# Kernel optimization log

Measured on AMD Instinct MI355X. Metric: run time of the kernel, lower is better.

## Reference

```python
import jax, jax.numpy as jnp
import numpy as np

N_HEAD = 8
D_HEAD = 32  # d_model=256 // n_head=8
SCALE = 1.0 / (D_HEAD ** 0.5)
CLIP = 10.0


def _rel_shift(x):
    # x: [qlen, klen, B, nh]; Transformer-XL relative shift along axis 1
    qlen, klen = x.shape[0], x.shape[1]
    zero_pad = jnp.zeros((qlen, 1) + x.shape[2:], dtype=x.dtype)
    x_pad = jnp.concatenate([zero_pad, x], axis=1)          # [qlen, klen+1, B, nh]
    x_pad = x_pad.reshape((klen + 1, qlen) + x.shape[2:])   # row-major reshape (torch .view)
    return x_pad[1:].reshape(x.shape)


def setup_inputs() -> dict:
    key = jax.random.key(0)
    ks = jax.random.split(key, 7)
    S, B, H = 1024, 8, 256
    return {
        "q": jax.random.normal(ks[0], (S, B, H), dtype=jnp.float32),
        "k": jax.random.normal(ks[1], (S, B, H), dtype=jnp.float32),
        "v": jax.random.normal(ks[2], (S, B, H), dtype=jnp.float32),
        "r": jax.random.normal(ks[3], (S, 1, H), dtype=jnp.float32),
        "bias_u": jax.random.normal(ks[4], (N_HEAD, D_HEAD), dtype=jnp.float32),
        "bias_v": jax.random.normal(ks[5], (N_HEAD, D_HEAD), dtype=jnp.float32),
        "mask": jax.random.randint(ks[6], (S, S, B), 0, 2).astype(jnp.bool_),
    }


def reference(q, k, v, r, bias_u, bias_v, mask):
    qlen, bsz = q.shape[0], q.shape[1]
    klen, rlen = k.shape[0], r.shape[0]
    q = q.reshape(qlen, bsz, N_HEAD, D_HEAD)
    k = k.reshape(klen, bsz, N_HEAD, D_HEAD)
    v = v.reshape(klen, bsz, N_HEAD, D_HEAD)
    r = r.reshape(rlen, N_HEAD, D_HEAD)

    AC = jnp.einsum('ibnd,jbnd->ijbn', q + bias_u, k)   # content term
    BD = jnp.einsum('ibnd,jnd->ijbn', q + bias_v, r)    # position term
    BD = _rel_shift(BD)

    score = (AC + BD) * SCALE
    score = CLIP * jnp.tanh(score)                      # clip > 0 path

    weight = jax.nn.softmax(score, axis=1)              # softmax over klen

    # mask is not None path: masked softmax of head-mean logits
    logits = score.mean(axis=-1)                        # [qlen, klen, B]
    logits = jnp.where(mask, -jnp.inf, logits)
    probs = jax.nn.softmax(logits, axis=1)

    out = jnp.einsum('ijbn,jbnd->ibnd', weight, v)
    out = out.reshape(qlen, bsz, N_HEAD * D_HEAD)
    return out, probs
```

## Files before the change

### kernel.cpp

```cpp
#include <hip/hip_runtime.h>
#include <hip/hip_fp16.h>

#define S 1024
#define B 8
#define NH 8
#define DH 32
#define HID 256
#define SCALEF 0.17677669529663687f

typedef __attribute__((ext_vector_type(8))) _Float16 f16x8;
typedef __attribute__((ext_vector_type(4))) _Float16 f16x4;
typedef __attribute__((ext_vector_type(4))) float f32x4;
#define MFMAH(a, b, c) __builtin_amdgcn_mfma_f32_16x16x32_f16(a, b, c, 0, 0, 0)

#define OFF_K   0
#define OFF_VT  2560
#define OFF_RL  5120
#define OFF_RH  10240
#define OFF_P   15360
#define LDS_HF  17920

#define C_E2  0.51006978f
#define C_PWA 14.42695041f
#define C_PWB -28.85390082f

__device__ __forceinline__ void cvtf16_4(const float4 x, _Float16* d) {
  f16x4 h;
  h.x = (_Float16)x.x; h.y = (_Float16)x.y; h.z = (_Float16)x.z; h.w = (_Float16)x.w;
  *(f16x4*)d = h;
}

__global__ __launch_bounds__(256)
void relattn_mfma_86028194939537(const float* __restrict__ q, const float* __restrict__ k,
                                 const float* __restrict__ v, const float* __restrict__ r,
                                 const float* __restrict__ bu, const float* __restrict__ bv,
                                 float* __restrict__ out, __half* __restrict__ sws) {
  __shared__ _Float16 sm[LDS_HF];
  const int t = threadIdx.x;
  const int lane = t & 63, w = t >> 6;
  const int quad = lane >> 4, jn = lane & 15;
  const int bid = blockIdx.x;
  const int b = bid & 7, it = (bid >> 3) & 15, n = bid >> 7;
  const int i0 = it << 6, iw0 = i0 + (w << 4);
  const int colq = quad << 3;
  const int i16 = i0 >> 4;

  const int jstage = t >> 3, dstage = (t & 7) << 2;
  const int jsw = jstage ^ ((t & 3) << 3);
  const int vcolsw = colq ^ (((jn >> 2) & 3) << 3);

  const int jtL_last = (i0 + 63) >> 5;
  const bool proH = (i0 <= 125);

  f16x8 qu_h, qu_l, qv_h, qv_l, qn_h, qn_l;
  {
    const float* bup = bu + n * DH + colq;
    const float* bvp = bv + n * DH + colq;
    const float* qp = q + (size_t)(iw0 + jn) * 2048 + b * HID + n * DH + colq;
    int r1 = iw0 + 1 + jn; if (r1 > S - 1) r1 = S - 1;
    const float* qp1 = q + (size_t)r1 * 2048 + b * HID + n * DH + colq;
#pragma unroll
    for (int e = 0; e < 8; ++e) {
      float xu = (qp[e] + bup[e]) * C_E2;
      float xv = (qp[e] + bvp[e]) * C_E2;
      float xn = (qp1[e] + bvp[e]) * C_E2;
      _Float16 h;
      h = (_Float16)xu; qu_h[e] = h; qu_l[e] = (_Float16)(xu - (float)h);
      h = (_Float16)xv; qv_h[e] = h; qv_l[e] = (_Float16)(xv - (float)h);
      h = (_Float16)xn; qn_h[e] = h; qn_l[e] = (_Float16)(xn - (float)h);
    }
  }

  f16x8 ones1;
#pragma unroll
  for (int e = 0; e < 8; ++e) ones1[e] = (_Float16)1.0f;

  __half* swsp = sws + (((size_t)(iw0 + jn) * 8 + b) * 8 + n) * 1024 + colq;

  f32x4 out0 = {0.f, 0.f, 0.f, 0.f}, out1 = {0.f, 0.f, 0.f, 0.f};
  f32x4 out_sum = {0.f, 0.f, 0.f, 0.f};

  {
    const size_t g = (size_t)jstage * 2048 + b * HID + n * DH + dstage;
    float4 kx = *(const float4*)(k + g);
    float4 vx = *(const float4*)(v + g);
    cvtf16_4(kx, &sm[OFF_K + jstage * 40 + dstage]);
    sm[OFF_VT + (dstage + 0) * 40 + jsw] = (_Float16)vx.x;
    sm[OFF_VT + (dstage + 1) * 40 + jsw] = (_Float16)vx.y;
    sm[OFF_VT + (dstage + 2) * 40 + jsw] = (_Float16)vx.z;
    sm[OFF_VT + (dstage + 3) * 40 + jsw] = (_Float16)vx.w;
  }
#pragma unroll
  for (int p = 0; p < 3; ++p) {
    int ti = 2 * p + (t >> 7), row = (t >> 3) & 15, d4 = (t & 7) << 2;
    {
      int kL = 60 - i16 + ti;
      int tg = (kL << 4) + row; tg = tg < 0 ? 0 : (tg > S - 1 ? S - 1 : tg);
      float4 rv = *(const float4*)(r + (size_t)tg * HID + n * DH + d4);
      int sl = (kL + 72) & 7;
      cvtf16_4(rv, &sm[OFF_RL + (sl * 16 + row) * 40 + d4]);
    }
    if (proH) {
      int kH = -i16 - 3 + ti;
      int tg = (kH << 4) - 17 + row; tg = tg < 0 ? 0 : (tg > S - 1 ? S - 1 : tg);
      float4 rv = *(const float4*)(r + (size_t)tg * HID + n * DH + d4);
      int sl = (kH + 72) & 7;
      cvtf16_4(rv, &sm[OFF_RH + (sl * 16 + row) * 40 + d4]);
    }
  }

  for (int jt = 0; jt < 32; ++jt) {
    const int j0 = jt << 5;
    __syncthreads();

    const bool doKV = (jt < 31);
    const bool doRL = (jt <= jtL_last);
    const bool doRH = (32 * jt >= i0 - 125);
    float4 kx, vx, rlv, rhv;
    int slL = 0, slH = 0;
    {
      if (doKV) {
        const size_t g = (size_t)(j0 + 32 + jstage) * 2048 + b * HID + n * DH + dstage;
        kx = *(const float4*)(k + g);
        vx = *(const float4*)(v + g);
      }
      const int ti = t >> 7, row = (t >> 3) & 15, d4r = (t & 7) << 2;
      if (doRL) {
        int kL = 66 + 2 * jt - i16 + ti;
        int tg = (kL << 4) + row; tg = tg < 0 ? 0 : (tg > S - 1 ? S - 1 : tg);
        rlv = *(const float4*)(r + (size_t)tg * HID + n * DH + d4r);
        slL = (kL + 72) & 7;
      }
      if (doRH) {
        int kH = 2 * jt - i16 + 3 + ti;
        int tg = (kH << 4) - 17 + row; tg = tg < 0 ? 0 : (tg > S - 1 ? S - 1 : tg);
        rhv = *(const float4*)(r + (size_t)tg * HID + n * DH + d4r);
        slH = (kH + 72) & 7;
      }
    }

    const int buf = (jt & 1) * 1280;
    const bool lowA = (j0 <= iw0 + 15);
    const bool highA = (j0 + 29 >= iw0);

    f32x4 ac0 = {0.f, 0.f, 0.f, 0.f}, ac1 = {0.f, 0.f, 0.f, 0.f};
    {
      f16x8 b0 = *(const f16x8*)&sm[OFF_K + buf + jn * 40 + colq];
      f16x8 b1 = *(const f16x8*)&sm[OFF_K + buf + (16 + jn) * 40 + colq];
      ac0 = MFMAH(qu_h, b0, ac0); ac0 = MFMAH(qu_l, b0, ac0);
      ac1 = MFMAH(qu_h, b1, ac1); ac1 = MFMAH(qu_l, b1, ac1);
    }

    f32x4 zl0 = {0.f,0.f,0.f,0.f}, zl1 = {0.f,0.f,0.f,0.f}, zl2 = {0.f,0.f,0.f,0.f};
    f32x4 zh0 = {0.f,0.f,0.f,0.f}, zh1 = {0.f,0.f,0.f,0.f}, zh2 = {0.f,0.f,0.f,0.f};
    if (lowA) {
#pragma unroll
      for (int z = 0; z < 3; ++z) {
        int kL = 63 - i16 - w + 2 * jt + z;
        int sl = (kL + 72) & 7;
        f16x8 rr = *(const f16x8*)&sm[OFF_RL + (sl * 16 + jn) * 40 + colq];
        f32x4 acc = {0.f, 0.f, 0.f, 0.f};
        acc = MFMAH(qv_h, rr, acc); acc = MFMAH(qv_l, rr, acc);
        if (z == 0) zl0 = acc; else if (z == 1) zl1 = acc; else zl2 = acc;
      }
    }
    if (highA) {
#pragma unroll
      for (int z = 0; z < 3; ++z) {
        int kH = 2 * jt - i16 - w + z;
        int sl = (kH + 72) & 7;
        f16x8 rr = *(const f16x8*)&sm[OFF_RH + (sl * 16 + jn) * 40 + colq];
        f32x4 acc = {0.f, 0.f, 0.f, 0.f};
        acc = MFMAH(qn_h, rr, acc); acc = MFMAH(qn_l, rr, acc);
        if (z == 0) zh0 = acc; else if (z == 1) zh1 = acc; else zh2 = acc;
      }
    }

#pragma unroll
    for (int g = 0; g < 4; ++g) {
      const int qr = (quad << 2) + g;
      const int c0 = 15 - qr + jn;
      const int src = (lane & 48) | (c0 & 15);
      const bool pred = (jn >= 15 - qr);
      float lo0 = 0.f, lo1 = 0.f, hv0 = 0.f, hv1 = 0.f;
      if (lowA) {
        float vA = pred ? zl0[g] : zl1[g];
        float vB = pred ? zl1[g] : zl2[g];
        lo0 = __shfl(vA, src, 64);
        lo1 = __shfl(vB, src, 64);
      }
      if (highA) {
        float vA = pred ? zh0[g] : zh1[g];
        float vB = pred ? zh1[g] : zh2[g];
        hv0 = __shfl(vA, src, 64);
        hv1 = __shfl(vB, src, 64);
      }
      const int dj0 = j0 + jn - iw0 - qr;
#pragma unroll
      for (int f = 0; f < 2; ++f) {
        const int dj = dj0 + (f << 4);
        const float bd = (dj <= 0) ? (f ? lo1 : lo0) : ((dj == 1) ? 0.f : (f ? hv1 : hv0));
        const float acv = f ? ac1[g] : ac0[g];
        const float s = acv + bd;
        const float e2 = __builtin_amdgcn_exp2f(s);
        const float tq = __builtin_amdgcn_rcpf(e2 + 1.f);
        const float pw = __builtin_amdgcn_exp2f(fmaf(tq, C_PWB, C_PWA));
        sm[OFF_P + w * 640 + qr * 40 + (f << 4) + jn] = (_Float16)pw;
      }
    }

    {
      f16x8 pa = *(const f16x8*)&sm[OFF_P + w * 640 + jn * 40 + colq];
      f16x8 v0 = *(const f16x8*)&sm[OFF_VT + buf + jn * 40 + vcolsw];
      f16x8 v1 = *(const f16x8*)&sm[OFF_VT + buf + (16 + jn) * 40 + vcolsw];
      out0 = MFMAH(pa, v0, out0);
      out1 = MFMAH(pa, v1, out1);
      out_sum = MFMAH(pa, ones1, out_sum);
      *(f16x8*)swsp = pa;
      swsp += 32;
    }

    {
      if (doKV) {
        const int nbuf = ((jt + 1) & 1) * 1280;
        cvtf16_4(kx, &sm[OFF_K + nbuf + jstage * 40 + dstage]);
        sm[OFF_VT + nbuf + (dstage + 0) * 40 + jsw] = (_Float16)vx.x;
        sm[OFF_VT + nbuf + (dstage + 1) * 40 + jsw] = (_Float16)vx.y;
        sm[OFF_VT + nbuf + (dstage + 2) * 40 + jsw] = (_Float16)vx.z;
        sm[OFF_VT + nbuf + (dstage + 3) * 40 + jsw] = (_Float16)vx.w;
      }
      const int row = (t >> 3) & 15, d4r = (t & 7) << 2;
      if (doRL) cvtf16_4(rlv, &sm[OFF_RL + (slL * 16 + row) * 40 + d4r]);
      if (doRH) cvtf16_4(rhv, &sm[OFF_RH + (slH * 16 + row) * 40 + d4r]);
    }
  }

#pragma unroll
  for (int g = 0; g < 4; ++g) {
    const float inv = 1.0f / out_sum[g];
    const int qr = (quad << 2) + g;
    float* op = out + (size_t)(iw0 + qr) * 2048 + b * HID + n * DH;
    op[jn] = out0[g] * inv;
    op[16 + jn] = out1[g] * inv;
  }
}

__global__ __launch_bounds__(1024)
void relattn_probs_86028194939537(const __half* __restrict__ sws, const int* __restrict__ mask,
                                  float* __restrict__ probs) {
  __shared__ _Float16 ebuf[8][1032];
  __shared__ unsigned char mb[9224];
  __shared__ float psum[8][4];
  __shared__ float binv[8];
  const int t = threadIdx.x;
  const int i = blockIdx.x;
  const int tj = t & 255, bg = t >> 8;
  const int j4 = tj << 2;
  const int wl = (t >> 6) & 3;

  {
    const int4* m4 = (const int4*)(mask + (size_t)i * 8192);
#pragma unroll
    for (int u = 0; u < 2; ++u) {
      int idx = t + (u << 10);
      int4 mv = m4[idx];
      int jj = idx >> 1, b0 = (idx & 1) << 2;
      mb[jj * 9 + b0 + 0] = (unsigned char)(mv.x != 0);
      mb[jj * 9 + b0 + 1] = (unsigned char)(mv.y != 0);
      mb[jj * 9 + b0 + 2] = (unsigned char)(mv.z != 0);
      mb[jj * 9 + b0 + 3] = (unsigned char)(mv.w != 0);
    }
  }
  __syncthreads();

#pragma unroll
  for (int bb = 0; bb < 2; ++bb) {
    const int b = (bg << 1) + bb;
    float a0 = 1.f, a1 = 1.f, a2 = 1.f, a3 = 1.f;
#pragma unroll
    for (int n = 0; n < 8; ++n) {
      f16x4 pv = *(const f16x4*)(sws + (((size_t)i * 8 + b) * 8 + n) * 1024 + j4);
      a0 *= (float)pv.x; a1 *= (float)pv.y; a2 *= (float)pv.z; a3 *= (float)pv.w;
    }
    float e0 = mb[(j4 + 0) * 9 + b] ? 0.f
             : __builtin_amdgcn_exp2f(0.125f * __builtin_amdgcn_logf(a0));
    float e1 = mb[(j4 + 1) * 9 + b] ? 0.f
             : __builtin_amdgcn_exp2f(0.125f * __builtin_amdgcn_logf(a1));
    float e2 = mb[(j4 + 2) * 9 + b] ? 0.f
             : __builtin_amdgcn_exp2f(0.125f * __builtin_amdgcn_logf(a2));
    float e3 = mb[(j4 + 3) * 9 + b] ? 0.f
             : __builtin_amdgcn_exp2f(0.125f * __builtin_amdgcn_logf(a3));
    f16x4 ev;
    ev.x = (_Float16)e0; ev.y = (_Float16)e1; ev.z = (_Float16)e2; ev.w = (_Float16)e3;
    *(f16x4*)&ebuf[b][j4] = ev;
    float s = ((float)ev.x + (float)ev.y) + ((float)ev.z + (float)ev.w);
#pragma unroll
    for (int off = 32; off > 0; off >>= 1) s += __shfl_xor(s, off, 64);
    if ((t & 63) == 0) psum[b][wl] = s;
  }
  __syncthreads();
  if (t < 8) binv[t] = 1.0f / (psum[t][0] + psum[t][1] + psum[t][2] + psum[t][3]);
  __syncthreads();
#pragma unroll
  for (int u = 0; u < 2; ++u) {
    int f0 = (t << 2) + (u << 12);
    float4 o;
    o.x = (float)ebuf[(f0 + 0) & 7][(f0 + 0) >> 3] * binv[(f0 + 0) & 7];
    o.y = (float)ebuf[(f0 + 1) & 7][(f0 + 1) >> 3] * binv[(f0 + 1) & 7];
    o.z = (float)ebuf[(f0 + 2) & 7][(f0 + 2) >> 3] * binv[(f0 + 2) & 7];
    o.w = (float)ebuf[(f0 + 3) & 7][(f0 + 3) >> 3] * binv[(f0 + 3) & 7];
    *(float4*)(probs + (size_t)i * 8192 + f0) = o;
  }
}

#define TI 8
#define TJ 8
#define NTILE (S / TJ)
#define KSTR 288
#define KOFF 0
#define VOFF (TJ * KSTR)
#define BAND (2 * TJ * KSTR)
#define PROWS (TI + TJ - 1)
#define BSTR 292
#define BVR (BAND + PROWS * BSTR)
#define BUKo (BVR + PROWS * 8)
#define LDS_FL (BUKo + 64)

__global__ __launch_bounds__(256, 2)
void relattn_main_fb(const float* __restrict__ q, const float* __restrict__ k,
                     const float* __restrict__ v, const float* __restrict__ r,
                     const float* __restrict__ bias_u, const float* __restrict__ bias_v,
                     const int* __restrict__ mask, float* __restrict__ out,
                     float* __restrict__ probs_raw, float* __restrict__ ws_logits, int use_ws) {
  __shared__ float smf[LDS_FL];
  const int t = threadIdx.x;
  const int n = t & 7;
  const int il = (t >> 3) & 7;
  const int jp = t >> 6;
  const int bid = blockIdx.x;
  const int b = bid & 7;
  const int i0 = (bid >> 3) * TI;
  const int i = i0 + il;
  float qq[DH], qn[DH];
  {
    const float4* qr = (const float4*)(q + (i * B + b) * HID + n * DH);
#pragma unroll
    for (int dd = 0; dd < 8; ++dd) {
      float4 a = qr[dd];
      qq[4*dd+0] = a.x; qq[4*dd+1] = a.y; qq[4*dd+2] = a.z; qq[4*dd+3] = a.w;
    }
    if (i + 1 < S) {
      const float4* q2 = (const float4*)(q + ((i + 1) * B + b) * HID + n * DH);
#pragma unroll
      for (int dd = 0; dd < 8; ++dd) {
        float4 a = q2[dd];
        qn[4*dd+0] = a.x; qn[4*dd+1] = a.y; qn[4*dd+2] = a.z; qn[4*dd+3] = a.w;
      }
    } else {
#pragma unroll
      for (int d = 0; d < DH; ++d) qn[d] = 0.f;
    }
  }
  float oacc[DH];
#pragma unroll
  for (int d = 0; d < DH; ++d) oacc[d] = 0.f;
  float lsum = 0.f;
  for (int jt = 0; jt < NTILE; ++jt) {
    const int j0 = jt * TJ;
    const int Pstar = i0 + (TI - 1) - j0;
    const int lowBase = S - TI + j0 - i0;
    const int upBase = j0 - i0 - (TI + 1);
    __syncthreads();
    {
      int u = t;
      int row = u >> 6, c = u & 63;
      int gofs = ((j0 + row) * B + b) * HID + c * 4;
      int lofs = row * KSTR + (c >> 3) * 36 + (c & 7) * 4;
      *(float4*)(smf + KOFF + lofs) = *(const float4*)(k + gofs);
      *(float4*)(smf + VOFF + lofs) = *(const float4*)(v + gofs);
      u = t + 256; row = u >> 6; c = u & 63;
      gofs = ((j0 + row) * B + b) * HID + c * 4;
      lofs = row * KSTR + (c >> 3) * 36 + (c & 7) * 4;
      *(float4*)(smf + KOFF + lofs) = *(const float4*)(k + gofs);
      *(float4*)(smf + VOFF + lofs) = *(const float4*)(v + gofs);
    }
    for (int u = t; u < PROWS * 64; u += 256) {
      int prow = u >> 6, c = u & 63;
      int trow = (prow <= Pstar) ? (lowBase + prow) : (upBase + prow);
      float4 val = make_float4(0.f, 0.f, 0.f, 0.f);
      if ((unsigned)trow < (unsigned)S) val = *(const float4*)(r + trow * HID + c * 4);
      *(float4*)(smf + BAND + prow * BSTR + (c >> 3) * 36 + (c & 7) * 4) = val;
    }
    if (t < 64 + PROWS * 8) {
      const float4 *bb, *src;
      int slot;
      bool zero = false;
      if (t < 64) {
        int jl = t >> 3, nn = t & 7;
        bb = (const float4*)(bias_u + nn * DH);
        src = (const float4*)(k + ((j0 + jl) * B + b) * HID + nn * DH);
        slot = BUKo + jl * 8 + nn;
      } else {
        int u2 = t - 64;
        int prow = u2 >> 3, nn = u2 & 7;
        int trow = (prow <= Pstar) ? (lowBase + prow) : (upBase + prow);
        bb = (const float4*)(bias_v + nn * DH);
        if ((unsigned)trow < (unsigned)S) src = (const float4*)(r + trow * HID + nn * DH);
        else { src = bb; zero = true; }
        slot = BVR + prow * 8 + nn;
      }
      float a0 = 0.f, a1 = 0.f, a2 = 0.f, a3 = 0.f;
#pragma unroll
      for (int dd = 0; dd < 8; ++dd) {
        float4 x = bb[dd], y = src[dd];
        a0 = fmaf(x.x, y.x, a0); a1 = fmaf(x.y, y.y, a1);
        a2 = fmaf(x.z, y.z, a2); a3 = fmaf(x.w, y.w, a3);
      }
      smf[slot] = zero ? 0.f : ((a0 + a1) + (a2 + a3));
    }
    __syncthreads();
#pragma unroll
    for (int jj = 0; jj < 2; ++jj) {
      const int jl = jp * 2 + jj;
      const int jg = j0 + jl;
      const int p = jl + (TI - 1) - il;
      float a0 = 0.f, a1 = 0.f, a2 = 0.f, a3 = 0.f;
      const float4* kr = (const float4*)(smf + KOFF + jl * KSTR + n * 36);
#pragma unroll
      for (int dd = 0; dd < 8; ++dd) {
        float4 kv = kr[dd];
        a0 = fmaf(qq[4*dd+0], kv.x, a0); a1 = fmaf(qq[4*dd+1], kv.y, a1);
        a2 = fmaf(qq[4*dd+2], kv.z, a2); a3 = fmaf(qq[4*dd+3], kv.w, a3);
      }
      float ac = (a0 + a1) + (a2 + a3) + smf[BUKo + jl * 8 + n];
      float b0 = 0.f, b1 = 0.f, b2 = 0.f, b3 = 0.f;
      const float4* br = (const float4*)(smf + BAND + p * BSTR + n * 36);
      if (jg <= i) {
#pragma unroll
        for (int dd = 0; dd < 8; ++dd) {
          float4 bv4 = br[dd];
          b0 = fmaf(qq[4*dd+0], bv4.x, b0); b1 = fmaf(qq[4*dd+1], bv4.y, b1);
          b2 = fmaf(qq[4*dd+2], bv4.z, b2); b3 = fmaf(qq[4*dd+3], bv4.w, b3);
        }
      } else {
#pragma unroll
        for (int dd = 0; dd < 8; ++dd) {
          float4 bv4 = br[dd];
          b0 = fmaf(qn[4*dd+0], bv4.x, b0); b1 = fmaf(qn[4*dd+1], bv4.y, b1);
          b2 = fmaf(qn[4*dd+2], bv4.z, b2); b3 = fmaf(qn[4*dd+3], bv4.w, b3);
        }
      }
      float bd = (b0 + b1) + (b2 + b3) + smf[BVR + p * 8 + n];
      float sr = (ac + bd) * SCALEF;
      sr = fminf(fmaxf(sr, -15.f), 15.f);
      float e2 = __expf(2.f * sr);
      float scv = 10.f * (e2 - 1.f) / (e2 + 1.f);
      float ssum = scv;
      ssum += __shfl_xor(ssum, 1, 64);
      ssum += __shfl_xor(ssum, 2, 64);
      ssum += __shfl_xor(ssum, 4, 64);
      if (n == 0) {
        float logit = ssum * 0.125f;
        if (use_ws) {
          ws_logits[(i * B + b) * S + jg] = logit;
        } else {
          int gofs = (i * S + jg) * B + b;
          probs_raw[gofs] = (mask[gofs] != 0) ? -1e30f : logit;
        }
      }
      float pw = __expf(scv);
      lsum += pw;
      const float4* vr = (const float4*)(smf + VOFF + jl * KSTR + n * 36);
#pragma unroll
      for (int dd = 0; dd < 8; ++dd) {
        float4 vv = vr[dd];
        oacc[4*dd+0] = fmaf(pw, vv.x, oacc[4*dd+0]);
        oacc[4*dd+1] = fmaf(pw, vv.y, oacc[4*dd+1]);
        oacc[4*dd+2] = fmaf(pw, vv.z, oacc[4*dd+2]);
        oacc[4*dd+3] = fmaf(pw, vv.w, oacc[4*dd+3]);
      }
    }
  }
  __syncthreads();
  if (jp >= 2) {
    float* red = smf + (t - 128) * 33;
#pragma unroll
    for (int d = 0; d < DH; ++d) red[d] = oacc[d];
    red[DH] = lsum;
  }
  __syncthreads();
  if (jp < 2) {
    const float* red = smf + t * 33;
#pragma unroll
    for (int d = 0; d < DH; ++d) oacc[d] += red[d];
    lsum += red[DH];
  }
  __syncthreads();
  if (jp == 1) {
    float* red = smf + (t - 64) * 33;
#pragma unroll
    for (int d = 0; d < DH; ++d) red[d] = oacc[d];
    red[DH] = lsum;
  }
  __syncthreads();
  if (jp == 0) {
    const float* red = smf + t * 33;
#pragma unroll
    for (int d = 0; d < DH; ++d) oacc[d] += red[d];
    lsum += red[DH];
    float inv = 1.f / lsum;
    float4* orow = (float4*)(out + (i * B + b) * HID + n * DH);
#pragma unroll
    for (int dd = 0; dd < 8; ++dd) {
      float4 o4;
      o4.x = oacc[4*dd+0] * inv; o4.y = oacc[4*dd+1] * inv;
      o4.z = oacc[4*dd+2] * inv; o4.w = oacc[4*dd+3] * inv;
      orow[dd] = o4;
    }
  }
}

__global__ __launch_bounds__(256)
void relattn_norm_fb(float* __restrict__ probs, const float* __restrict__ ws_logits,
                     const int* __restrict__ mask, int use_ws) {
  const int t = threadIdx.x;
  const int bid = blockIdx.x;
  const int b = bid & 7;
  const int i = bid >> 3;
  float vals[4];
  float s = 0.f;
#pragma unroll
  for (int kk = 0; kk < 4; ++kk) {
    int j = t + 256 * kk;
    float lg;
    if (use_ws) {
      lg = ws_logits[(i * B + b) * S + j];
      if (mask[(i * S + j) * B + b] != 0) lg = -1e30f;
    } else {
      lg = probs[(i * S + j) * B + b];
    }
    vals[kk] = __expf(lg);
    s += vals[kk];
  }
#pragma unroll
  for (int off = 32; off > 0; off >>= 1) s += __shfl_down(s, off, 64);
  __shared__ float wsum[4];
  __shared__ float tot;
  if ((t & 63) == 0) wsum[t >> 6] = s;
  __syncthreads();
  if (t == 0) tot = wsum[0] + wsum[1] + wsum[2] + wsum[3];
  __syncthreads();
  float inv = 1.f / tot;
#pragma unroll
  for (int kk = 0; kk < 4; ++kk) {
    int j = t + 256 * kk;
    probs[(i * S + j) * B + b] = vals[kk] * inv;
  }
}

extern "C" void kernel_launch(void* const* d_in, const int* in_sizes, int n_in,
                              void* d_out, int out_size, void* d_ws, size_t ws_size,
                              hipStream_t stream) {
  const float* q  = (const float*)d_in[0];
  const float* k  = (const float*)d_in[1];
  const float* v  = (const float*)d_in[2];
  const float* r  = (const float*)d_in[3];
  const float* bu = (const float*)d_in[4];
  const float* bv = (const float*)d_in[5];
  const int* mask = (const int*)d_in[6];
  float* out = (float*)d_out;
  float* probs = out + S * B * HID;

  const size_t WS_NEED = (size_t)S * S * B * NH * sizeof(__half);
  if (ws_size >= WS_NEED) {
    __half* sws = (__half*)d_ws;
    relattn_mfma_86028194939537<<<dim3(1024), dim3(256), 0, stream>>>(
        q, k, v, r, bu, bv, out, sws);
    relattn_probs_86028194939537<<<dim3(1024), dim3(1024), 0, stream>>>(sws, mask, probs);
  } else {
    float* wsl = (float*)d_ws;
    const int use_ws = (ws_size >= (size_t)S * S * B * sizeof(float)) ? 1 : 0;
    relattn_main_fb<<<dim3((S / TI) * B), dim3(256), 0, stream>>>(
        q, k, v, r, bu, bv, mask, out, probs, wsl, use_ws);
    relattn_norm_fb<<<dim3(S * B), dim3(256), 0, stream>>>(probs, wsl, mask, use_ws);
  }
}
```

Before: 247.0 us.

## Fuse attention and probs kernels with flag-based cross-block row handoff

Replaces the two-kernel path with one persistent-style kernel of 512 blocks. Each block computes two attention tiles, then signals per-64-row completion flags and dynamically pulls probs rows from an atomic counter, spinning until the producing tiles are done. A cleanup kernel handles rows whose wait timed out. The aim is to overlap the probs softmax with the attention tail and remove the launch gap, at the cost of spin-wait, atomics and reliance on co-residency. The probs computation is also rewritten to use 256 threads per row, with the mask staged in LDS.

```diff
diff --git a/kernel.cpp b/kernel.cpp
--- a/kernel.cpp
+++ b/kernel.cpp
@@ -24,10 +24,356 @@
 #define C_PWA 14.42695041f
 #define C_PWB -28.85390082f
 
+#define CTRL_INTS 1042
+
 __device__ __forceinline__ void cvtf16_4(const float4 x, _Float16* d) {
   f16x4 h;
   h.x = (_Float16)x.x; h.y = (_Float16)x.y; h.z = (_Float16)x.z; h.w = (_Float16)x.w;
   *(f16x4*)d = h;
+}
+
+__device__ __forceinline__ void probs_row_256(
+    int i, const __half* __restrict__ sws, const int* __restrict__ mask,
+    float* __restrict__ probs, _Float16* ebuf, unsigned char* mb,
+    float* psum, float* binv) {
+  const int t = threadIdx.x;
+  {
+    const int4* m4 = (const int4*)(mask + (size_t)i * 8192);
+#pragma unroll
+    for (int uu = 0; uu < 8; ++uu) {
+      int idx = t + (uu << 8);
+      int4 mv = m4[idx];
+      int jj = idx >> 1, b0 = (idx & 1) << 2;
+      mb[jj * 9 + b0 + 0] = (unsigned char)(mv.x != 0);
+      mb[jj * 9 + b0 + 1] = (unsigned char)(mv.y != 0);
+      mb[jj * 9 + b0 + 2] = (unsigned char)(mv.z != 0);
+      mb[jj * 9 + b0 + 3] = (unsigned char)(mv.w != 0);
+    }
+  }
+  __syncthreads();
+  const int b = t >> 5, g32 = t & 31;
+  float s = 0.f;
+#pragma unroll
+  for (int rep = 0; rep < 8; ++rep) {
+    const int j4 = (g32 + (rep << 5)) << 2;
+    float a0 = 1.f, a1 = 1.f, a2 = 1.f, a3 = 1.f;
+#pragma unroll
+    for (int n = 0; n < 8; ++n) {
+      f16x4 pv = *(const f16x4*)(sws + (((size_t)i * 8 + b) * 8 + n) * 1024 + j4);
+      a0 *= (float)pv.x; a1 *= (float)pv.y; a2 *= (float)pv.z; a3 *= (float)pv.w;
+    }
+    float e0 = mb[(j4 + 0) * 9 + b] ? 0.f
+             : __builtin_amdgcn_exp2f(0.125f * __builtin_amdgcn_logf(a0));
+    float e1 = mb[(j4 + 1) * 9 + b] ? 0.f
+             : __builtin_amdgcn_exp2f(0.125f * __builtin_amdgcn_logf(a1));
+    float e2 = mb[(j4 + 2) * 9 + b] ? 0.f
+             : __builtin_amdgcn_exp2f(0.125f * __builtin_amdgcn_logf(a2));
+    float e3 = mb[(j4 + 3) * 9 + b] ? 0.f
+             : __builtin_amdgcn_exp2f(0.125f * __builtin_amdgcn_logf(a3));
+    f16x4 ev;
+    ev.x = (_Float16)e0; ev.y = (_Float16)e1; ev.z = (_Float16)e2; ev.w = (_Float16)e3;
+    *(f16x4*)&ebuf[b * 1032 + j4] = ev;
+    s += ((float)ev.x + (float)ev.y) + ((float)ev.z + (float)ev.w);
+  }
+#pragma unroll
+  for (int off = 16; off > 0; off >>= 1) s += __shfl_xor(s, off, 64);
+  if (g32 == 0) psum[b] = s;
+  __syncthreads();
+  if (t < 8) binv[t] = 1.0f / psum[t];
+  __syncthreads();
+#pragma unroll
+  for (int uu = 0; uu < 8; ++uu) {
+    int f0 = (t << 2) + (uu << 10);
+    float4 o;
+    o.x = (float)ebuf[((f0 + 0) & 7) * 1032 + ((f0 + 0) >> 3)] * binv[(f0 + 0) & 7];
+    o.y = (float)ebuf[((f0 + 1) & 7) * 1032 + ((f0 + 1) >> 3)] * binv[(f0 + 1) & 7];
+    o.z = (float)ebuf[((f0 + 2) & 7) * 1032 + ((f0 + 2) >> 3)] * binv[(f0 + 2) & 7];
+    o.w = (float)ebuf[((f0 + 3) & 7) * 1032 + ((f0 + 3) >> 3)] * binv[(f0 + 3) & 7];
+    *(float4*)(probs + (size_t)i * 8192 + f0) = o;
+  }
+}
+
+__global__ __launch_bounds__(1024)
+void relattn_init_ctrl(int* __restrict__ ctrl) {
+  int t = threadIdx.x + blockIdx.x * 1024;
+  if (t < CTRL_INTS) ctrl[t] = 0;
+}
+
+__global__ __launch_bounds__(256)
+void relattn_fused_86028194939537(const float* __restrict__ q, const float* __restrict__ k,
+                                  const float* __restrict__ v, const float* __restrict__ r,
+                                  const float* __restrict__ bu, const float* __restrict__ bv,
+                                  const int* __restrict__ mask, float* __restrict__ out,
+                                  float* __restrict__ probs, __half* __restrict__ sws,
+                                  int* __restrict__ ctrl) {
+  __shared__ _Float16 sm[LDS_HF];
+  __shared__ float psum[8];
+  __shared__ float binv[8];
+  __shared__ int smrow;
+  __shared__ int smok;
+  const int t = threadIdx.x;
+  const int lane = t & 63, w = t >> 6;
+  const int quad = lane >> 4, jn = lane & 15;
+  const int colq = quad << 3;
+  const int jstage = t >> 3, dstage = (t & 7) << 2;
+  const int jsw = jstage ^ ((t & 3) << 3);
+  const int vcolsw = colq ^ (((jn >> 2) & 3) << 3);
+
+  int* flags = ctrl;
+  int* rowctr = ctrl + 16;
+  int* lcnt = ctrl + 17;
+  int* lrows = ctrl + 18;
+
+#pragma unroll 1
+  for (int uu = 0; uu < 2; ++uu) {
+    const int u = 2 * (int)blockIdx.x + uu;
+    const int it = u >> 6, n = (u >> 3) & 7, b = u & 7;
+    const int i0 = it << 6, iw0 = i0 + (w << 4);
+    const int i16 = i0 >> 4;
+    const int jtL_last = (i0 + 63) >> 5;
+    const bool proH = (i0 <= 125);
+
+    f16x8 qu_h, qu_l, qv_h, qv_l, qn_h, qn_l;
+    {
+      const float* bup = bu + n * DH + colq;
+      const float* bvp = bv + n * DH + colq;
+      const float* qp = q + (size_t)(iw0 + jn) * 2048 + b * HID + n * DH + colq;
+      int r1 = iw0 + 1 + jn; if (r1 > S - 1) r1 = S - 1;
+      const float* qp1 = q + (size_t)r1 * 2048 + b * HID + n * DH + colq;
+#pragma unroll
+      for (int e = 0; e < 8; ++e) {
+        float xu = (qp[e] + bup[e]) * C_E2;
+        float xv = (qp[e] + bvp[e]) * C_E2;
+        float xn = (qp1[e] + bvp[e]) * C_E2;
+        _Float16 h;
+        h = (_Float16)xu; qu_h[e] = h; qu_l[e] = (_Float16)(xu - (float)h);
+        h = (_Float16)xv; qv_h[e] = h; qv_l[e] = (_Float16)(xv - (float)h);
+        h = (_Float16)xn; qn_h[e] = h; qn_l[e] = (_Float16)(xn - (float)h);
+      }
+    }
+    f16x8 ones1;
+#pragma unroll
+    for (int e = 0; e < 8; ++e) ones1[e] = (_Float16)1.0f;
+
+    __half* swsp = sws + (((size_t)(iw0 + jn) * 8 + b) * 8 + n) * 1024 + colq;
+
+    f32x4 out0 = {0.f, 0.f, 0.f, 0.f}, out1 = {0.f, 0.f, 0.f, 0.f};
+    f32x4 out_sum = {0.f, 0.f, 0.f, 0.f};
+
+    __syncthreads();
+    {
+      const size_t g = (size_t)jstage * 2048 + b * HID + n * DH + dstage;
+      float4 kx = *(const float4*)(k + g);
+      float4 vx = *(const float4*)(v + g);
+      cvtf16_4(kx, &sm[OFF_K + jstage * 40 + dstage]);
+      sm[OFF_VT + (dstage + 0) * 40 + jsw] = (_Float16)vx.x;
+      sm[OFF_VT + (dstage + 1) * 40 + jsw] = (_Float16)vx.y;
+      sm[OFF_VT + (dstage + 2) * 40 + jsw] = (_Float16)vx.z;
+      sm[OFF_VT + (dstage + 3) * 40 + jsw] = (_Float16)vx.w;
+    }
+#pragma unroll
+    for (int p = 0; p < 3; ++p) {
+      int ti = 2 * p + (t >> 7), row = (t >> 3) & 15, d4 = (t & 7) << 2;
+      {
+        int kL = 60 - i16 + ti;
+        int tg = (kL << 4) + row; tg = tg < 0 ? 0 : (tg > S - 1 ? S - 1 : tg);
+        float4 rv = *(const float4*)(r + (size_t)tg * HID + n * DH + d4);
+        int sl = (kL + 72) & 7;
+        cvtf16_4(rv, &sm[OFF_RL + (sl * 16 + row) * 40 + d4]);
+      }
+      if (proH) {
+        int kH = -i16 - 3 + ti;
+        int tg = (kH << 4) - 17 + row; tg = tg < 0 ? 0 : (tg > S - 1 ? S - 1 : tg);
+        float4 rv = *(const float4*)(r + (size_t)tg * HID + n * DH + d4);
+        int sl = (kH + 72) & 7;
+        cvtf16_4(rv, &sm[OFF_RH + (sl * 16 + row) * 40 + d4]);
+      }
+    }
+
+    for (int jt = 0; jt < 32; ++jt) {
+      const int j0 = jt << 5;
+      __syncthreads();
+
+      const bool doKV = (jt < 31);
+      const bool doRL = (jt <= jtL_last);
+      const bool doRH = (32 * jt >= i0 - 125);
+      float4 kx, vx, rlv, rhv;
+      int slL = 0, slH = 0;
+      {
+        if (doKV) {
+          const size_t g = (size_t)(j0 + 32 + jstage) * 2048 + b * HID + n * DH + dstage;
+          kx = *(const float4*)(k + g);
+          vx = *(const float4*)(v + g);
+        }
+        const int ti = t >> 7, row = (t >> 3) & 15, d4r = (t & 7) << 2;
+        if (doRL) {
+          int kL = 66 + 2 * jt - i16 + ti;
+          int tg = (kL << 4) + row; tg = tg < 0 ? 0 : (tg > S - 1 ? S - 1 : tg);
+          rlv = *(const float4*)(r + (size_t)tg * HID + n * DH + d4r);
+          slL = (kL + 72) & 7;
+        }
+        if (doRH) {
+          int kH = 2 * jt - i16 + 3 + ti;
+          int tg = (kH << 4) - 17 + row; tg = tg < 0 ? 0 : (tg > S - 1 ? S - 1 : tg);
+          rhv = *(const float4*)(r + (size_t)tg * HID + n * DH + d4r);
+          slH = (kH + 72) & 7;
+        }
+      }
+
+      const int buf = (jt & 1) * 1280;
+      const bool lowA = (j0 <= iw0 + 15);
+      const bool highA = (j0 + 29 >= iw0);
+
+      f32x4 ac0 = {0.f, 0.f, 0.f, 0.f}, ac1 = {0.f, 0.f, 0.f, 0.f};
+      {
+        f16x8 b0 = *(const f16x8*)&sm[OFF_K + buf + jn * 40 + colq];
+        f16x8 b1 = *(const f16x8*)&sm[OFF_K + buf + (16 + jn) * 40 + colq];
+        ac0 = MFMAH(qu_h, b0, ac0); ac0 = MFMAH(qu_l, b0, ac0);
+        ac1 = MFMAH(qu_h, b1, ac1); ac1 = MFMAH(qu_l, b1, ac1);
+      }
+
+      f32x4 zl0 = {0.f,0.f,0.f,0.f}, zl1 = {0.f,0.f,0.f,0.f}, zl2 = {0.f,0.f,0.f,0.f};
+      f32x4 zh0 = {0.f,0.f,0.f,0.f}, zh1 = {0.f,0.f,0.f,0.f}, zh2 = {0.f,0.f,0.f,0.f};
+      if (lowA) {
+#pragma unroll
+        for (int z = 0; z < 3; ++z) {
+          int kL = 63 - i16 - w + 2 * jt + z;
+          int sl = (kL + 72) & 7;
+          f16x8 rr = *(const f16x8*)&sm[OFF_RL + (sl * 16 + jn) * 40 + colq];
+          f32x4 acc = {0.f, 0.f, 0.f, 0.f};
+          acc = MFMAH(qv_h, rr, acc); acc = MFMAH(qv_l, rr, acc);
+          if (z == 0) zl0 = acc; else if (z == 1) zl1 = acc; else zl2 = acc;
+        }
+      }
+      if (highA) {
+#pragma unroll
+        for (int z = 0; z < 3; ++z) {
+          int kH = 2 * jt - i16 - w + z;
+          int sl = (kH + 72) & 7;
+          f16x8 rr = *(const f16x8*)&sm[OFF_RH + (sl * 16 + jn) * 40 + colq];
+          f32x4 acc = {0.f, 0.f, 0.f, 0.f};
+          acc = MFMAH(qn_h, rr, acc); acc = MFMAH(qn_l, rr, acc);
+          if (z == 0) zh0 = acc; else if (z == 1) zh1 = acc; else zh2 = acc;
+        }
+      }
+
+#pragma unroll
+      for (int g = 0; g < 4; ++g) {
+        const int qr = (quad << 2) + g;
+        const int c0 = 15 - qr + jn;
+        const int src = (lane & 48) | (c0 & 15);
+        const bool pred = (jn >= 15 - qr);
+        float lo0 = 0.f, lo1 = 0.f, hv0 = 0.f, hv1 = 0.f;
+        if (lowA) {
+          float vA = pred ? zl0[g] : zl1[g];
+          float vB = pred ? zl1[g] : zl2[g];
+          lo0 = __shfl(vA, src, 64);
+          lo1 = __shfl(vB, src, 64);
+        }
+        if (highA) {
+          float vA = pred ? zh0[g] : zh1[g];
+          float vB = pred ? zh1[g] : zh2[g];
+          hv0 = __shfl(vA, src, 64);
+          hv1 = __shfl(vB, src, 64);
+        }
+        const int dj0 = j0 + jn - iw0 - qr;
+#pragma unroll
+        for (int f = 0; f < 2; ++f) {
+          const int dj = dj0 + (f << 4);
+          const float bd = (dj <= 0) ? (f ? lo1 : lo0) : ((dj == 1) ? 0.f : (f ? hv1 : hv0));
+          const float acv = f ? ac1[g] : ac0[g];
+          const float sc = acv + bd;
+          const float e2 = __builtin_amdgcn_exp2f(sc);
+          const float tq = __builtin_amdgcn_rcpf(e2 + 1.f);
+          const float pw = __builtin_amdgcn_exp2f(fmaf(tq, C_PWB, C_PWA));
+          sm[OFF_P + w * 640 + qr * 40 + (f << 4) + jn] = (_Float16)pw;
+        }
+      }
+
+      {
+        f16x8 pa = *(const f16x8*)&sm[OFF_P + w * 640 + jn * 40 + colq];
+        f16x8 v0 = *(const f16x8*)&sm[OFF_VT + buf + jn * 40 + vcolsw];
+        f16x8 v1 = *(const f16x8*)&sm[OFF_VT + buf + (16 + jn) * 40 + vcolsw];
+        out0 = MFMAH(pa, v0, out0);
+        out1 = MFMAH(pa, v1, out1);
+        out_sum = MFMAH(pa, ones1, out_sum);
+        *(f16x8*)swsp = pa;
+        swsp += 32;
+      }
+
+      {
+        if (doKV) {
+          const int nbuf = ((jt + 1) & 1) * 1280;
+          cvtf16_4(kx, &sm[OFF_K + nbuf + jstage * 40 + dstage]);
+          sm[OFF_VT + nbuf + (dstage + 0) * 40 + jsw] = (_Float16)vx.x;
+          sm[OFF_VT + nbuf + (dstage + 1) * 40 + jsw] = (_Float16)vx.y;
+          sm[OFF_VT + nbuf + (dstage + 2) * 40 + jsw] = (_Float16)vx.z;
+          sm[OFF_VT + nbuf + (dstage + 3) * 40 + jsw] = (_Float16)vx.w;
+        }
+        const int row = (t >> 3) & 15, d4r = (t & 7) << 2;
+        if (doRL) cvtf16_4(rlv, &sm[OFF_RL + (slL * 16 + row) * 40 + d4r]);
+        if (doRH) cvtf16_4(rhv, &sm[OFF_RH + (slH * 16 + row) * 40 + d4r]);
+      }
+    }
+
+#pragma unroll
+    for (int g = 0; g < 4; ++g) {
+      const float inv = 1.0f / out_sum[g];
+      const int qr = (quad << 2) + g;
+      float* op = out + (size_t)(iw0 + qr) * 2048 + b * HID + n * DH;
+      op[jn] = out0[g] * inv;
+      op[16 + jn] = out1[g] * inv;
+    }
+
+    __syncthreads();
+    if (t == 0) {
+      __threadfence();
+      __hip_atomic_fetch_add(&flags[it], 1, __ATOMIC_RELEASE, __HIP_MEMORY_SCOPE_AGENT);
+    }
+  }
+
+  for (;;) {
+    if (t == 0)
+      smrow = __hip_atomic_fetch_add(rowctr, 1, __ATOMIC_RELAXED, __HIP_MEMORY_SCOPE_AGENT);
+    __syncthreads();
+    const int row = smrow;
+    if (row >= S) break;
+    const int st = row >> 6;
+    if (t == 0) {
+      int ok = 0;
+      for (int sp = 0; sp < 20000; ++sp) {
+        if (__hip_atomic_load(&flags[st], __ATOMIC_RELAXED, __HIP_MEMORY_SCOPE_AGENT) >= 64) {
+          ok = 1; break;
+        }
+        __builtin_amdgcn_s_sleep(8);
+      }
+      if (ok) {
+        (void)__hip_atomic_load(&flags[st], __ATOMIC_ACQUIRE, __HIP_MEMORY_SCOPE_AGENT);
+      } else {
+        int li = __hip_atomic_fetch_add(lcnt, 1, __ATOMIC_RELAXED, __HIP_MEMORY_SCOPE_AGENT);
+        lrows[li] = row;
+        __threadfence();
+      }
+      smok = ok;
+    }
+    __syncthreads();
+    if (!smok) continue;
+    probs_row_256(row, sws, mask, probs, sm, (unsigned char*)(sm + 8704), psum, binv);
+    __syncthreads();
+  }
+}
+
+__global__ __launch_bounds__(256)
+void relattn_cleanup_86028194939537(const __half* __restrict__ sws, const int* __restrict__ mask,
+                                    float* __restrict__ probs, const int* __restrict__ ctrl) {
+  __shared__ _Float16 ebuf[8 * 1032];
+  __shared__ unsigned char mb[9224];
+  __shared__ float psum[8];
+  __shared__ float binv[8];
+  const int cnt = ctrl[17];
+  if ((int)blockIdx.x >= cnt) return;
+  const int row = ctrl[18 + blockIdx.x];
+  probs_row_256(row, sws, mask, probs, ebuf, mb, psum, binv);
 }
 
 __global__ __launch_bounds__(256)
@@ -44,11 +390,9 @@
   const int i0 = it << 6, iw0 = i0 + (w << 4);
   const int colq = quad << 3;
   const int i16 = i0 >> 4;
-
   const int jstage = t >> 3, dstage = (t & 7) << 2;
   const int jsw = jstage ^ ((t & 3) << 3);
   const int vcolsw = colq ^ (((jn >> 2) & 3) << 3);
-
   const int jtL_last = (i0 + 63) >> 5;
   const bool proH = (i0 <= 125);
 
@@ -70,7 +414,6 @@
       h = (_Float16)xn; qn_h[e] = h; qn_l[e] = (_Float16)(xn - (float)h);
     }
   }
-
   f16x8 ones1;
 #pragma unroll
   for (int e = 0; e < 8; ++e) ones1[e] = (_Float16)1.0f;
@@ -201,8 +544,8 @@
         const int dj = dj0 + (f << 4);
         const float bd = (dj <= 0) ? (f ? lo1 : lo0) : ((dj == 1) ? 0.f : (f ? hv1 : hv0));
         const float acv = f ? ac1[g] : ac0[g];
-        const float s = acv + bd;
-        const float e2 = __builtin_amdgcn_exp2f(s);
+        const float sc = acv + bd;
+        const float e2 = __builtin_amdgcn_exp2f(sc);
         const float tq = __builtin_amdgcn_rcpf(e2 + 1.f);
         const float pw = __builtin_amdgcn_exp2f(fmaf(tq, C_PWB, C_PWA));
         sm[OFF_P + w * 640 + qr * 40 + (f << 4) + jn] = (_Float16)pw;
@@ -571,8 +914,18 @@
   float* out = (float*)d_out;
   float* probs = out + S * B * HID;
 
-  const size_t WS_NEED = (size_t)S * S * B * NH * sizeof(__half);
-  if (ws_size >= WS_NEED) {
+  const size_t WS_SWS = (size_t)S * S * B * NH * sizeof(__half);
+  const size_t WS_FUSED = WS_SWS + 8192;
+
+  if (ws_size >= WS_FUSED) {
+    __half* sws = (__half*)d_ws;
+    int* ctrl = (int*)((char*)d_ws + WS_SWS);
+    relattn_init_ctrl<<<dim3(2), dim3(1024), 0, stream>>>(ctrl);
+    relattn_fused_86028194939537<<<dim3(512), dim3(256), 0, stream>>>(
+        q, k, v, r, bu, bv, mask, out, probs, sws, ctrl);
+    relattn_cleanup_86028194939537<<<dim3(1024), dim3(256), 0, stream>>>(
+        sws, mask, probs, ctrl);
+  } else if (ws_size >= WS_SWS) {
     __half* sws = (__half*)d_ws;
     relattn_mfma_86028194939537<<<dim3(1024), dim3(256), 0, stream>>>(
         q, k, v, r, bu, bv, out, sws);
```

Result: slower. 347.9 us (+40.9%).
